# Optimization experiments

Measured on AMD Instinct MI355X. Metric: run time of the kernel, lower is better.

The kernel has to match this reference:

```python
import jax, jax.numpy as jnp
import numpy as np

B, T, C, H, WIN = 1, 2048, 512, 8, 48
DH = C // H  # 64


def setup_inputs() -> dict:
    key = jax.random.key(0)
    kx, kq, ko, kp = jax.random.split(key, 4)
    x = jax.random.normal(kx, (B, T, C), dtype=jnp.float32)
    W_qkv = jax.random.normal(kq, (C, 3 * C), dtype=jnp.float32) / np.sqrt(C).astype(np.float32)
    W_out = jax.random.normal(ko, (C, C), dtype=jnp.float32) / np.sqrt(C).astype(np.float32)
    # one random cycle permutation per head: perms[h, pi_pos] = original_pos
    perms = jax.vmap(lambda k: jax.random.permutation(k, T))(jax.random.split(kp, H)).astype(jnp.int32)
    return {"x": x, "W_qkv": W_qkv, "W_out": W_out, "perms": perms}


def _head_attn(qh, kh, vh, perm):
    # qh, kh, vh: [B, T, DH]; perm: [T] with perm[pi_pos] = original_pos
    Tn = perm.shape[0]
    inv_perm = jnp.argsort(perm)  # inv_perm[orig_pos] = pi_pos
    q_pi = qh[:, perm]
    k_pi = kh[:, perm]
    v_pi = vh[:, perm]
    offs = jnp.arange(-WIN, WIN + 1)                      # [W]
    pi_idx = jnp.arange(Tn)[:, None] + offs[None, :]      # [T, W]
    idx = jnp.clip(pi_idx, 0, Tn - 1)
    k_win = k_pi[:, idx]                                  # [B, T, W, DH]
    v_win = v_pi[:, idx]                                  # [B, T, W, DH]
    scores = jnp.einsum('btd,btwd->btw', q_pi, k_win) / np.sqrt(DH).astype(np.float32)
    neigh_orig = perm[idx]                                # [T, W] original positions of neighbors
    mask = (neigh_orig <= perm[:, None]) & (pi_idx >= 0) & (pi_idx < Tn)  # causal + window validity
    scores = jnp.where(mask[None], scores, jnp.finfo(scores.dtype).min)
    w = jax.nn.softmax(scores, axis=-1)                   # [B, T, W]
    y_pi = jnp.einsum('btw,btwd->btd', w, v_win)          # [B, T, DH]
    return y_pi[:, inv_perm]                              # back to original order


def reference(x, W_qkv, W_out, perms):
    qkv = x @ W_qkv                                       # [B, T, 3C]
    q, k, v = jnp.split(qkv, 3, axis=-1)
    q = q.reshape(B, T, H, DH)
    k = k.reshape(B, T, H, DH)
    v = v.reshape(B, T, H, DH)
    # heads are independent; vmap over head axis with per-head permutation
    y = jax.vmap(_head_attn, in_axes=(2, 2, 2, 0), out_axes=2)(q, k, v, perms)  # [B, T, H, DH]
    return y.reshape(B, T, C) @ W_out
```

## Files before the change

### kernel.cpp

```cpp
#include <hip/hip_runtime.h>
#include <float.h>
#include <math.h>

#define T_DIM 2048
#define C_DIM 512
#define QKV_LD 1536
#define NBLK 512

typedef float f32x4 __attribute__((ext_vector_type(4)));
typedef short s16x8 __attribute__((ext_vector_type(8)));

__device__ __forceinline__ unsigned short f2bf(float f) {
  unsigned u = __float_as_uint(f);
  return (unsigned short)((u + 0x7fffu + ((u >> 16) & 1u)) >> 16);
}

__device__ __forceinline__ void load16_to_lds(const void* g, void* l) {
  __builtin_amdgcn_global_load_lds(
      (const __attribute__((address_space(1))) unsigned int*)g,
      (__attribute__((address_space(3))) unsigned int*)(unsigned int)(unsigned long long)l,
      16, 0, 0);
}

__global__ __launch_bounds__(256) void prep_kernel(const float* __restrict__ x,
                                                   const float* __restrict__ Wqkv,
                                                   const float* __restrict__ Wout,
                                                   unsigned short* __restrict__ xbf,
                                                   unsigned short* __restrict__ WqkvT,
                                                   unsigned short* __restrict__ WoutT) {
  __shared__ float tile[32][33];
  const int tid = threadIdx.x, bid = blockIdx.x;

  const float4* xs4 = (const float4*)x;
  for (int i = bid * 256 + tid; i < (T_DIM * C_DIM) / 4; i += NBLK * 256) {
    float4 v = xs4[i];
    ushort4 o;
    o.x = f2bf(v.x); o.y = f2bf(v.y); o.z = f2bf(v.z); o.w = f2bf(v.w);
    ((ushort4*)xbf)[i] = o;
  }
  const int tx = tid & 31, ty = tid >> 5;
  for (int tt = bid; tt < 1024; tt += NBLK) {
    const float* src; unsigned short* dst; int Cc, R, bx, by;
    if (tt < 768) { src = Wqkv; dst = WqkvT; Cc = QKV_LD; R = C_DIM; bx = (tt % 48) * 32; by = (tt / 48) * 32; }
    else { int u = tt - 768; src = Wout; dst = WoutT; Cc = C_DIM; R = C_DIM; bx = (u & 15) * 32; by = (u >> 4) * 32; }
    __syncthreads();
#pragma unroll
    for (int i = 0; i < 4; ++i) { int r = ty + i * 8; tile[r][tx] = src[(size_t)(by + r) * Cc + bx + tx]; }
    __syncthreads();
#pragma unroll
    for (int i = 0; i < 4; ++i) { int r = ty + i * 8; dst[(size_t)(bx + r) * R + by + tx] = f2bf(tile[tx][r]); }
  }
}

template <int BM, int BN, bool OUT16>
__device__ __forceinline__ void gemm_body(const unsigned short* __restrict__ A,
                                          const unsigned short* __restrict__ BT,
                                          void* __restrict__ Cp,
                                          int N, int K, int tilesX,
                                          unsigned short* lA, unsigned short* lB,
                                          int tid, int bid) {
  constexpr int BK = 32;
  constexpr int BM2 = BM / 2, BN2 = BN / 2;
  constexpr int MT = BM2 / 16, NT = BN2 / 16;
  constexpr int IA = BM / 64;
  constexpr int IB = BN / 64;
  const int lane = tid & 63, w = tid >> 6, wr = w >> 1, wc = w & 1;
  const int fm = lane & 15, q8 = (lane >> 4) * 8, q4 = lane >> 4;

  const int m0 = (bid / tilesX) * BM, n0 = (bid % tilesX) * BN;
  f32x4 acc[MT][NT] = {};
  for (int k0 = 0; k0 < K; k0 += BK) {
    __syncthreads();
#pragma unroll
    for (int i = 0; i < IA; ++i) {
      int c = i * 256 + tid, row = c >> 2, c8 = (c & 3) * 8;
      load16_to_lds(&A[(size_t)(m0 + row) * K + k0 + c8], lA + c * 8);
    }
#pragma unroll
    for (int i = 0; i < IB; ++i) {
      int c = i * 256 + tid, row = c >> 2, c8 = (c & 3) * 8;
      load16_to_lds(&BT[(size_t)(n0 + row) * K + k0 + c8], lB + c * 8);
    }
    __syncthreads();
    s16x8 a[MT], b[NT];
#pragma unroll
    for (int mi = 0; mi < MT; ++mi)
      a[mi] = *(const s16x8*)&lA[(wr * BM2 + mi * 16 + fm) * BK + q8];
#pragma unroll
    for (int ni = 0; ni < NT; ++ni)
      b[ni] = *(const s16x8*)&lB[(wc * BN2 + ni * 16 + fm) * BK + q8];
#pragma unroll
    for (int mi = 0; mi < MT; ++mi)
#pragma unroll
      for (int ni = 0; ni < NT; ++ni)
        acc[mi][ni] = __builtin_amdgcn_mfma_f32_16x16x32_bf16(a[mi], b[ni], acc[mi][ni], 0, 0, 0);
  }
#pragma unroll
  for (int mi = 0; mi < MT; ++mi)
#pragma unroll
    for (int ni = 0; ni < NT; ++ni)
#pragma unroll
      for (int r = 0; r < 4; ++r) {
        int row = m0 + wr * BM2 + mi * 16 + q4 * 4 + r;
        int col = n0 + wc * BN2 + ni * 16 + fm;
        if constexpr (OUT16)
          ((unsigned short*)Cp)[(size_t)row * N + col] = f2bf(acc[mi][ni][r]);
        else
          ((float*)Cp)[(size_t)row * N + col] = acc[mi][ni][r];
      }
}

__global__ __launch_bounds__(256) void gemm1_kernel(const unsigned short* __restrict__ A,
                                                    const unsigned short* __restrict__ BT,
                                                    unsigned short* __restrict__ Cc) {
  __shared__ __align__(16) unsigned short smem[(128 + 128) * 32];
  gemm_body<128, 128, true>(A, BT, Cc, QKV_LD, C_DIM, 12, smem, smem + 128 * 32,
                            threadIdx.x, blockIdx.x);
}
__global__ __launch_bounds__(256) void gemm2_kernel(const unsigned short* __restrict__ A,
                                                    const unsigned short* __restrict__ BT,
                                                    float* __restrict__ Cc) {
  __shared__ __align__(16) unsigned short smem[(64 + 64) * 32];
  gemm_body<64, 64, false>(A, BT, Cc, C_DIM, C_DIM, 8, smem, smem + 64 * 32,
                           threadIdx.x, blockIdx.x);
}

__global__ __launch_bounds__(256) void attn_kernel(const unsigned short* __restrict__ qkvbf,
                                                   const int* __restrict__ perms,
                                                   unsigned short* __restrict__ Ybf) {
  __shared__ __align__(16) unsigned char smem[48768];
  int* ow            = (int*)smem;
  unsigned short* lQ = (unsigned short*)(smem + 512);
  unsigned short* lK = (unsigned short*)(smem + 5120);
  float* Sb          = (float*)(smem + 23552);
  unsigned short* lP = (unsigned short*)(smem + 40064);
  unsigned short* lVT= (unsigned short*)(smem + 5120);

  const int tid = threadIdx.x, bid = blockIdx.x;
  const int lane = tid & 63, w = tid >> 6;
  const int fm = lane & 15, q8 = (lane >> 4) * 8, q4 = lane >> 4;
  const int h = bid >> 6;
  const int t0 = (bid & 63) << 5;

  if (tid < 128) {
    int pi = t0 - 48 + tid;
    int idx = min(max(pi, 0), T_DIM - 1);
    ow[tid] = perms[h * T_DIM + idx];
  }
  __syncthreads();

#pragma unroll
  for (int it = 0; it < 4; ++it) {
    int c = it * 256 + tid;
    int row = c >> 3, k8 = c & 7;
    uint4 d = *(const uint4*)(qkvbf + (size_t)ow[row] * QKV_LD + C_DIM + h * 64 + k8 * 8);
    *(uint4*)(lK + row * 72 + k8 * 8) = d;
  }
  {
    int row = tid >> 3, k8 = tid & 7;
    uint4 d = *(const uint4*)(qkvbf + (size_t)ow[48 + row] * QKV_LD + h * 64 + k8 * 8);
    *(uint4*)(lQ + row * 72 + k8 * 8) = d;
  }
  __syncthreads();

  {
    f32x4 accs[2][2] = {};
#pragma unroll
    for (int kt = 0; kt < 2; ++kt) {
      s16x8 aq[2];
#pragma unroll
      for (int mi = 0; mi < 2; ++mi)
        aq[mi] = *(const s16x8*)&lQ[(mi * 16 + fm) * 72 + kt * 32 + q8];
#pragma unroll
      for (int ni = 0; ni < 2; ++ni) {
        s16x8 bk = *(const s16x8*)&lK[(w * 32 + ni * 16 + fm) * 72 + kt * 32 + q8];
#pragma unroll
        for (int mi = 0; mi < 2; ++mi)
          accs[mi][ni] = __builtin_amdgcn_mfma_f32_16x16x32_bf16(aq[mi], bk, accs[mi][ni], 0, 0, 0);
      }
    }
#pragma unroll
    for (int mi = 0; mi < 2; ++mi)
#pragma unroll
      for (int ni = 0; ni < 2; ++ni)
#pragma unroll
        for (int r = 0; r < 4; ++r)
          Sb[(mi * 16 + q4 * 4 + r) * 129 + w * 32 + ni * 16 + fm] = accs[mi][ni][r] * 0.125f;
  }
  __syncthreads();

#pragma unroll
  for (int it = 0; it < 2; ++it) {
    int c2 = it * 256 + tid;
    int r = c2 & 63, d0 = (c2 >> 6) * 8;
    uint4 va = *(const uint4*)(qkvbf + (size_t)ow[2 * r]     * QKV_LD + 2 * C_DIM + h * 64 + d0);
    uint4 vb = *(const uint4*)(qkvbf + (size_t)ow[2 * r + 1] * QKV_LD + 2 * C_DIM + h * 64 + d0);
    *(unsigned*)(lVT + (d0 + 0) * 136 + 2 * r) = (va.x & 0xffffu) | (vb.x << 16);
    *(unsigned*)(lVT + (d0 + 1) * 136 + 2 * r) = (va.x >> 16) | (vb.x & 0xffff0000u);
    *(unsigned*)(lVT + (d0 + 2) * 136 + 2 * r) = (va.y & 0xffffu) | (vb.y << 16);
    *(unsigned*)(lVT + (d0 + 3) * 136 + 2 * r) = (va.y >> 16) | (vb.y & 0xffff0000u);
    *(unsigned*)(lVT + (d0 + 4) * 136 + 2 * r) = (va.z & 0xffffu) | (vb.z << 16);
    *(unsigned*)(lVT + (d0 + 5) * 136 + 2 * r) = (va.z >> 16) | (vb.z & 0xffff0000u);
    *(unsigned*)(lVT + (d0 + 6) * 136 + 2 * r) = (va.w & 0xffffu) | (vb.w << 16);
    *(unsigned*)(lVT + (d0 + 7) * 136 + 2 * r) = (va.w >> 16) | (vb.w & 0xffff0000u);
  }

  for (int si = 0; si < 8; ++si) {
    const int s = w * 8 + si;
    const int p = ow[48 + s];
    const int c1 = lane + 64;
    const float v0 = Sb[s * 129 + lane];
    const float v1 = Sb[s * 129 + c1];
    const int pi0 = t0 - 48 + lane;
    const bool valid0 = (lane >= s) && (pi0 >= 0) && (pi0 < T_DIM) && (ow[lane] <= p);
    const bool valid1 = (lane <= s + 32) && (pi0 + 64 < T_DIM) && (ow[c1] <= p);
    float mx = fmaxf(valid0 ? v0 : -FLT_MAX, valid1 ? v1 : -FLT_MAX);
#pragma unroll
    for (int off = 32; off > 0; off >>= 1) mx = fmaxf(mx, __shfl_xor(mx, off, 64));
    const float e0 = valid0 ? __expf(v0 - mx) : 0.f;
    const float e1 = valid1 ? __expf(v1 - mx) : 0.f;
    float sum = e0 + e1;
#pragma unroll
    for (int off = 32; off > 0; off >>= 1) sum += __shfl_xor(sum, off, 64);
    const float inv = 1.f / sum;
    lP[s * 136 + lane] = valid0 ? f2bf(e0 * inv) : (unsigned short)0;
    lP[s * 136 + c1]   = valid1 ? f2bf(e1 * inv) : (unsigned short)0;
  }
  __syncthreads();

  {
    const int wr = w >> 1, wc = w & 1;
    f32x4 acco[2] = {};
#pragma unroll
    for (int kt = 0; kt < 4; ++kt) {
      s16x8 ap = *(const s16x8*)&lP[(wr * 16 + fm) * 136 + kt * 32 + q8];
#pragma unroll
      for (int ni = 0; ni < 2; ++ni) {
        s16x8 bv = *(const s16x8*)&lVT[((wc * 2 + ni) * 16 + fm) * 136 + kt * 32 + q8];
        acco[ni] = __builtin_amdgcn_mfma_f32_16x16x32_bf16(ap, bv, acco[ni], 0, 0, 0);
      }
    }
#pragma unroll
    for (int ni = 0; ni < 2; ++ni)
#pragma unroll
      for (int r = 0; r < 4; ++r) {
        int q = wr * 16 + q4 * 4 + r;
        int d = (wc * 2 + ni) * 16 + fm;
        Ybf[(size_t)ow[48 + q] * C_DIM + h * 64 + d] = f2bf(acco[ni][r]);
      }
  }
}

extern "C" void kernel_launch(void* const* d_in, const int* in_sizes, int n_in,
                              void* d_out, int out_size, void* d_ws, size_t ws_size,
                              hipStream_t stream) {
  const float* x     = (const float*)d_in[0];
  const float* Wqkv  = (const float*)d_in[1];
  const float* Wout  = (const float*)d_in[2];
  const int*   perms = (const int*)d_in[3];
  float* out = (float*)d_out;
  unsigned short* ws = (unsigned short*)d_ws;

  unsigned short* xbf   = ws;
  unsigned short* WqkvT = xbf + 1048576;
  unsigned short* WoutT = WqkvT + 786432;
  unsigned short* qkvbf = WoutT + 262144;
  unsigned short* Ybf   = qkvbf + 3145728;

  prep_kernel<<<NBLK, 256, 0, stream>>>(x, Wqkv, Wout, xbf, WqkvT, WoutT);
  gemm1_kernel<<<192, 256, 0, stream>>>(xbf, WqkvT, qkvbf);
  attn_kernel<<<NBLK, 256, 0, stream>>>(qkvbf, perms, Ybf);
  gemm2_kernel<<<256, 256, 0, stream>>>(Ybf, WoutT, out);
}
```

Measured before the change: 96.66 us.

## Double-buffer GEMM LDS tiles and prefetch V before QK^T in attention

The shared GEMM body now keeps two LDS buffers and issues the async global-to-LDS loads for the next K tile before computing the current one, with one barrier per iteration instead of two. In the attention kernel, the gathered V rows are loaded into registers before the QK^T MFMA phase and written transposed into LDS afterwards, so global latency overlaps the score computation. This doubles GEMM shared memory and raises register pressure in the attention kernel.

Measured after the change: 93.29 us. 1.04x faster.

```diff
diff --git a/kernel.cpp b/kernel.cpp
--- a/kernel.cpp
+++ b/kernel.cpp
@@ -60,6 +60,7 @@
                                           unsigned short* lA, unsigned short* lB,
                                           int tid, int bid) {
   constexpr int BK = 32;
+  constexpr int ASZ = BM * BK, BSZ = BN * BK;
   constexpr int BM2 = BM / 2, BN2 = BN / 2;
   constexpr int MT = BM2 / 16, NT = BN2 / 16;
   constexpr int IA = BM / 64;
@@ -68,27 +69,39 @@
   const int fm = lane & 15, q8 = (lane >> 4) * 8, q4 = lane >> 4;
 
   const int m0 = (bid / tilesX) * BM, n0 = (bid % tilesX) * BN;
-  f32x4 acc[MT][NT] = {};
-  for (int k0 = 0; k0 < K; k0 += BK) {
-    __syncthreads();
+
+  auto stage = [&](int t, int buf) {
+    const int k0 = t * BK;
+    unsigned short* dA = lA + buf * ASZ;
+    unsigned short* dB = lB + buf * BSZ;
 #pragma unroll
     for (int i = 0; i < IA; ++i) {
       int c = i * 256 + tid, row = c >> 2, c8 = (c & 3) * 8;
-      load16_to_lds(&A[(size_t)(m0 + row) * K + k0 + c8], lA + c * 8);
+      load16_to_lds(&A[(size_t)(m0 + row) * K + k0 + c8], dA + c * 8);
     }
 #pragma unroll
     for (int i = 0; i < IB; ++i) {
       int c = i * 256 + tid, row = c >> 2, c8 = (c & 3) * 8;
-      load16_to_lds(&BT[(size_t)(n0 + row) * K + k0 + c8], lB + c * 8);
-    }
+      load16_to_lds(&BT[(size_t)(n0 + row) * K + k0 + c8], dB + c * 8);
+    }
+  };
+
+  f32x4 acc[MT][NT] = {};
+  const int nt = K / BK;
+  stage(0, 0);
+  for (int t = 0; t < nt; ++t) {
+    const int cur = t & 1;
     __syncthreads();
+    if (t + 1 < nt) stage(t + 1, cur ^ 1);
+    const unsigned short* sA = lA + cur * ASZ;
+    const unsigned short* sB = lB + cur * BSZ;
     s16x8 a[MT], b[NT];
 #pragma unroll
     for (int mi = 0; mi < MT; ++mi)
-      a[mi] = *(const s16x8*)&lA[(wr * BM2 + mi * 16 + fm) * BK + q8];
+      a[mi] = *(const s16x8*)&sA[(wr * BM2 + mi * 16 + fm) * BK + q8];
 #pragma unroll
     for (int ni = 0; ni < NT; ++ni)
-      b[ni] = *(const s16x8*)&lB[(wc * BN2 + ni * 16 + fm) * BK + q8];
+      b[ni] = *(const s16x8*)&sB[(wc * BN2 + ni * 16 + fm) * BK + q8];
 #pragma unroll
     for (int mi = 0; mi < MT; ++mi)
 #pragma unroll
@@ -113,15 +126,15 @@
 __global__ __launch_bounds__(256) void gemm1_kernel(const unsigned short* __restrict__ A,
                                                     const unsigned short* __restrict__ BT,
                                                     unsigned short* __restrict__ Cc) {
-  __shared__ __align__(16) unsigned short smem[(128 + 128) * 32];
-  gemm_body<128, 128, true>(A, BT, Cc, QKV_LD, C_DIM, 12, smem, smem + 128 * 32,
+  __shared__ __align__(16) unsigned short smem[2 * (128 + 128) * 32];
+  gemm_body<128, 128, true>(A, BT, Cc, QKV_LD, C_DIM, 12, smem, smem + 2 * 128 * 32,
                             threadIdx.x, blockIdx.x);
 }
 __global__ __launch_bounds__(256) void gemm2_kernel(const unsigned short* __restrict__ A,
                                                     const unsigned short* __restrict__ BT,
                                                     float* __restrict__ Cc) {
-  __shared__ __align__(16) unsigned short smem[(64 + 64) * 32];
-  gemm_body<64, 64, false>(A, BT, Cc, C_DIM, C_DIM, 8, smem, smem + 64 * 32,
+  __shared__ __align__(16) unsigned short smem[2 * (64 + 64) * 32];
+  gemm_body<64, 64, false>(A, BT, Cc, C_DIM, C_DIM, 8, smem, smem + 2 * 64 * 32,
                            threadIdx.x, blockIdx.x);
 }
 
@@ -161,48 +174,56 @@
     uint4 d = *(const uint4*)(qkvbf + (size_t)ow[48 + row] * QKV_LD + h * 64 + k8 * 8);
     *(uint4*)(lQ + row * 72 + k8 * 8) = d;
   }
-  __syncthreads();
-
-  {
-    f32x4 accs[2][2] = {};
-#pragma unroll
-    for (int kt = 0; kt < 2; ++kt) {
-      s16x8 aq[2];
-#pragma unroll
-      for (int mi = 0; mi < 2; ++mi)
-        aq[mi] = *(const s16x8*)&lQ[(mi * 16 + fm) * 72 + kt * 32 + q8];
-#pragma unroll
-      for (int ni = 0; ni < 2; ++ni) {
-        s16x8 bk = *(const s16x8*)&lK[(w * 32 + ni * 16 + fm) * 72 + kt * 32 + q8];
-#pragma unroll
-        for (int mi = 0; mi < 2; ++mi)
-          accs[mi][ni] = __builtin_amdgcn_mfma_f32_16x16x32_bf16(aq[mi], bk, accs[mi][ni], 0, 0, 0);
-      }
-    }
-#pragma unroll
-    for (int mi = 0; mi < 2; ++mi)
-#pragma unroll
-      for (int ni = 0; ni < 2; ++ni)
-#pragma unroll
-        for (int r = 0; r < 4; ++r)
-          Sb[(mi * 16 + q4 * 4 + r) * 129 + w * 32 + ni * 16 + fm] = accs[mi][ni][r] * 0.125f;
-  }
-  __syncthreads();
-
+
+  uint4 va[2], vb[2];
 #pragma unroll
   for (int it = 0; it < 2; ++it) {
     int c2 = it * 256 + tid;
     int r = c2 & 63, d0 = (c2 >> 6) * 8;
-    uint4 va = *(const uint4*)(qkvbf + (size_t)ow[2 * r]     * QKV_LD + 2 * C_DIM + h * 64 + d0);
-    uint4 vb = *(const uint4*)(qkvbf + (size_t)ow[2 * r + 1] * QKV_LD + 2 * C_DIM + h * 64 + d0);
-    *(unsigned*)(lVT + (d0 + 0) * 136 + 2 * r) = (va.x & 0xffffu) | (vb.x << 16);
-    *(unsigned*)(lVT + (d0 + 1) * 136 + 2 * r) = (va.x >> 16) | (vb.x & 0xffff0000u);
-    *(unsigned*)(lVT + (d0 + 2) * 136 + 2 * r) = (va.y & 0xffffu) | (vb.y << 16);
-    *(unsigned*)(lVT + (d0 + 3) * 136 + 2 * r) = (va.y >> 16) | (vb.y & 0xffff0000u);
-    *(unsigned*)(lVT + (d0 + 4) * 136 + 2 * r) = (va.z & 0xffffu) | (vb.z << 16);
-    *(unsigned*)(lVT + (d0 + 5) * 136 + 2 * r) = (va.z >> 16) | (vb.z & 0xffff0000u);
-    *(unsigned*)(lVT + (d0 + 6) * 136 + 2 * r) = (va.w & 0xffffu) | (vb.w << 16);
-    *(unsigned*)(lVT + (d0 + 7) * 136 + 2 * r) = (va.w >> 16) | (vb.w & 0xffff0000u);
+    va[it] = *(const uint4*)(qkvbf + (size_t)ow[2 * r]     * QKV_LD + 2 * C_DIM + h * 64 + d0);
+    vb[it] = *(const uint4*)(qkvbf + (size_t)ow[2 * r + 1] * QKV_LD + 2 * C_DIM + h * 64 + d0);
+  }
+  __syncthreads();
+
+  {
+    f32x4 accs[2][2] = {};
+#pragma unroll
+    for (int kt = 0; kt < 2; ++kt) {
+      s16x8 aq[2];
+#pragma unroll
+      for (int mi = 0; mi < 2; ++mi)
+        aq[mi] = *(const s16x8*)&lQ[(mi * 16 + fm) * 72 + kt * 32 + q8];
+#pragma unroll
+      for (int ni = 0; ni < 2; ++ni) {
+        s16x8 bk = *(const s16x8*)&lK[(w * 32 + ni * 16 + fm) * 72 + kt * 32 + q8];
+#pragma unroll
+        for (int mi = 0; mi < 2; ++mi)
+          accs[mi][ni] = __builtin_amdgcn_mfma_f32_16x16x32_bf16(aq[mi], bk, accs[mi][ni], 0, 0, 0);
+      }
+    }
+#pragma unroll
+    for (int mi = 0; mi < 2; ++mi)
+#pragma unroll
+      for (int ni = 0; ni < 2; ++ni)
+#pragma unroll
+        for (int r = 0; r < 4; ++r)
+          Sb[(mi * 16 + q4 * 4 + r) * 129 + w * 32 + ni * 16 + fm] = accs[mi][ni][r] * 0.125f;
+  }
+  __syncthreads();
+
+#pragma unroll
+  for (int it = 0; it < 2; ++it) {
+    int c2 = it * 256 + tid;
+    int r = c2 & 63, d0 = (c2 >> 6) * 8;
+    uint4 a4 = va[it], b4 = vb[it];
+    *(unsigned*)(lVT + (d0 + 0) * 136 + 2 * r) = (a4.x & 0xffffu) | (b4.x << 16);
+    *(unsigned*)(lVT + (d0 + 1) * 136 + 2 * r) = (a4.x >> 16) | (b4.x & 0xffff0000u);
+    *(unsigned*)(lVT + (d0 + 2) * 136 + 2 * r) = (a4.y & 0xffffu) | (b4.y << 16);
+    *(unsigned*)(lVT + (d0 + 3) * 136 + 2 * r) = (a4.y >> 16) | (b4.y & 0xffff0000u);
+    *(unsigned*)(lVT + (d0 + 4) * 136 + 2 * r) = (a4.z & 0xffffu) | (b4.z << 16);
+    *(unsigned*)(lVT + (d0 + 5) * 136 + 2 * r) = (a4.z >> 16) | (b4.z & 0xffff0000u);
+    *(unsigned*)(lVT + (d0 + 6) * 136 + 2 * r) = (a4.w & 0xffffu) | (b4.w << 16);
+    *(unsigned*)(lVT + (d0 + 7) * 136 + 2 * r) = (a4.w >> 16) | (b4.w & 0xffff0000u);
   }
 
   for (int si = 0; si < 8; ++si) {
```
